# Kernel optimization log

Measured on AMD Instinct MI355X. Metric: run time of the kernel, lower is better.

Reference implementation:

```python
import jax, jax.numpy as jnp
import numpy as np

NUM_HEADS = 8


def setup_inputs() -> dict:
    key = jax.random.key(0)
    ks = jax.random.split(key, 12)
    b, c, h, w = 2, 256, 64, 64
    pe = 128  # palette_embed
    E = c
    s = 0.02
    return {
        "x": jax.random.normal(ks[0], (b, c, h, w), jnp.float32),
        "palette": jax.random.normal(ks[1], (b, pe, h, w), jnp.float32),
        "Wq": s * jax.random.normal(ks[2], (E, pe), jnp.float32),
        "bq": jnp.zeros((E,), jnp.float32),
        "Wk": s * jax.random.normal(ks[3], (E, E), jnp.float32),
        "bk": jnp.zeros((E,), jnp.float32),
        "Wv": s * jax.random.normal(ks[4], (E, E), jnp.float32),
        "bv": jnp.zeros((E,), jnp.float32),
        "Wo": s * jax.random.normal(ks[5], (E, E), jnp.float32),
        "bo": jnp.zeros((E,), jnp.float32),
    }


def reference(x, palette, Wq, bq, Wk, bk, Wv, bv, Wo, bo):
    b, c, h, w = x.shape
    E = c
    H = NUM_HEADS
    hd = E // H
    scale = hd ** -0.5

    # x: (b,c,h,w) -> (S, b, E)
    x_flat = x.reshape(b, c, h * w).transpose(2, 0, 1)
    k = x_flat @ Wk.T + bk  # (S, b, E)
    v = x_flat @ Wv.T + bv

    bp, cp, hp, wp = palette.shape
    p_flat = palette.reshape(bp, cp, hp * wp).transpose(2, 0, 1)  # (Sp, b, cp)
    q = p_flat @ Wq.T + bq  # (Sp, b, E)

    # Faithful to torch .view on (S,b,E)-contiguous tensors: flatten in that
    # memory order, then reshape to (b, L, H, hd) and move heads forward.
    def to_heads(t):
        return t.reshape(b, -1, H, hd).transpose(0, 2, 1, 3)  # (b, H, L, hd)

    qh, kh, vh = to_heads(q), to_heads(k), to_heads(v)

    scores = jnp.einsum("bhqd,bhkd->bhqk", qh, kh) * scale  # (b,H,Lq,Lk)
    attn = jax.nn.softmax(scores, axis=-1)
    out = jnp.einsum("bhqk,bhkd->bhqd", attn, vh)  # (b,H,Lq,hd)

    out = out.transpose(0, 2, 1, 3).reshape(b, -1, E)  # (b, Lq, E)
    out = out @ Wo.T + bo
    out = out.transpose(0, 2, 1).reshape(b, c, h, w)
    return x + out
```

## Files before the change

### kernel.cpp

```cpp
#include <hip/hip_runtime.h>

typedef unsigned int u32;
typedef unsigned short u16;
typedef __bf16 bf16x8 __attribute__((ext_vector_type(8)));
typedef float f32x4 __attribute__((ext_vector_type(4)));
typedef u32 u32x4 __attribute__((ext_vector_type(4)));
typedef u16 u16x4 __attribute__((ext_vector_type(4)));
typedef u16 u16x8 __attribute__((ext_vector_type(8)));

#define LOG2E 1.4426950408889634f
#define QSCALE 0.17677669529663687f

extern "C" __device__ float __ocml_native_exp2_f32(float);

__device__ __forceinline__ u16 f2bf(float f) {
  return __builtin_bit_cast(u16, static_cast<__bf16>(f));
}
__device__ __forceinline__ float bf2f(u16 u) {
  return __builtin_bit_cast(float, (u32)u << 16);
}
__device__ __forceinline__ u32 cvtpk(float lo, float hi) {
  u32 r;
  asm("v_cvt_pk_bf16_f32 %0, %1, %2" : "=v"(r) : "v"(lo), "v"(hi));
  return r;
}

__device__ __forceinline__ bf16x8 ldb8(const u16* p) {
  return __builtin_bit_cast(bf16x8, *(const u32x4*)p);
}

__device__ __forceinline__ f32x4 mfma16(bf16x8 a, bf16x8 b, f32x4 c) {
  return __builtin_amdgcn_mfma_f32_16x16x32_bf16(a, b, c, 0, 0, 0);
}

typedef __attribute__((address_space(3))) void lds_void;
typedef const __attribute__((address_space(1))) void gbl_void;
__device__ __forceinline__ void gl16(const void* g, void* l) {
  __builtin_amdgcn_global_load_lds((gbl_void*)g, (lds_void*)l, 16, 0, 0);
}

__global__ __launch_bounds__(256) void wconv(
    const float* __restrict__ wq, const float* __restrict__ wk,
    const float* __restrict__ wv, const float* __restrict__ wo,
    u16* __restrict__ dst) {
  int e4 = blockIdx.x * 256 + threadIdx.x;
  const float* src; int base;
  if (e4 < 8192)        { src = wq; base = 0; }
  else if (e4 < 24576)  { src = wk; base = 32768;  e4 -= 8192; }
  else if (e4 < 40960)  { src = wv; base = 98304;  e4 -= 24576; }
  else                  { src = wo; base = 163840; e4 -= 40960; }
  f32x4 v = *(const f32x4*)(src + e4 * 4);
  u16x4 r = { f2bf(v[0]), f2bf(v[1]), f2bf(v[2]), f2bf(v[3]) };
  *(u16x4*)(dst + base + e4 * 4) = r;
}

__global__ __launch_bounds__(256, 2) void qkv_proj(
    const float* __restrict__ x, const float* __restrict__ pal,
    const u16* __restrict__ wq, const u16* __restrict__ wk, const u16* __restrict__ wv,
    const float* __restrict__ bq, const float* __restrict__ bk, const float* __restrict__ bv,
    u16* __restrict__ qb, u16* __restrict__ kb, u16* __restrict__ vtg) {
  __shared__ alignas(16) u16 Xt[32 * 264];
  __shared__ alignas(16) u16 Pt[32 * 136];
  const int t = threadIdx.x;
  const int g0 = blockIdx.x * 32;
  const int s0 = g0 >> 1;
#pragma unroll
  for (int pass = 0; pass < 8; ++pass) {
    int c = pass * 256 + t;
    int row = c >> 2;
    int sc = (c & 3) * 4;
    f32x4 v = *(const f32x4*)(x + row * 4096 + s0 + sc);
#pragma unroll
    for (int i = 0; i < 4; ++i)
      Xt[(2 * (sc + i) + (row >> 8)) * 264 + (row & 255)] = f2bf(v[i]);
  }
#pragma unroll
  for (int pass = 0; pass < 4; ++pass) {
    int c = pass * 256 + t;
    int row = c >> 2;
    int sc = (c & 3) * 4;
    f32x4 v = *(const f32x4*)(pal + row * 4096 + s0 + sc);
#pragma unroll
    for (int i = 0; i < 4; ++i)
      Pt[(2 * (sc + i) + (row >> 7)) * 136 + (row & 127)] = f2bf(v[i]);
  }
  __syncthreads();

  const int lane = t & 63, w = t >> 6;
  const int c16 = lane & 15, g16 = lane >> 4;
  const int rtok = (w & 1) * 16 + c16;
  const int ntb = (w >> 1) * 8 + blockIdx.y * 4;
  const int B2 = g0 >> 12;
  const int l0 = (g0 & 4095) + (w & 1) * 16 + g16 * 4;

  bf16x8 ax[8], ap[4];
#pragma unroll
  for (int ks = 0; ks < 8; ++ks) ax[ks] = ldb8(&Xt[rtok * 264 + ks * 32 + g16 * 8]);
#pragma unroll
  for (int ks = 0; ks < 4; ++ks) ap[ks] = ldb8(&Pt[rtok * 136 + ks * 32 + g16 * 8]);

#pragma unroll 1
  for (int nt = ntb; nt < ntb + 4; ++nt) {
    const int e = nt * 16 + c16;
    const int hh = e >> 5, d = e & 31;
    const int bh = B2 * 8 + hh;
    f32x4 acc = {0.f, 0.f, 0.f, 0.f};
#pragma unroll
    for (int ks = 0; ks < 4; ++ks)
      acc = mfma16(ap[ks], ldb8(&wq[e * 128 + ks * 32 + g16 * 8]), acc);
    {
      float bb_ = bq[e];
      u16* dstq = qb + bh * 131072 + d;
#pragma unroll
      for (int j = 0; j < 4; ++j)
        dstq[(l0 + j) * 32] = f2bf((acc[j] + bb_) * (QSCALE * LOG2E));
    }
    acc = (f32x4){0.f, 0.f, 0.f, 0.f};
#pragma unroll
    for (int ks = 0; ks < 8; ++ks)
      acc = mfma16(ax[ks], ldb8(&wk[e * 256 + ks * 32 + g16 * 8]), acc);
    {
      float bb_ = bk[e];
      u16* dstk = kb + bh * 131072 + d;
#pragma unroll
      for (int j = 0; j < 4; ++j)
        dstk[(l0 + j) * 32] = f2bf(acc[j] + bb_);
    }
    acc = (f32x4){0.f, 0.f, 0.f, 0.f};
#pragma unroll
    for (int ks = 0; ks < 8; ++ks)
      acc = mfma16(ax[ks], ldb8(&wv[e * 256 + ks * 32 + g16 * 8]), acc);
    {
      float bb_ = bv[e];
      u16x4 pk = { f2bf(acc[0] + bb_), f2bf(acc[1] + bb_),
                   f2bf(acc[2] + bb_), f2bf(acc[3] + bb_) };
      *(u16x4*)&vtg[(bh * 32 + d) * 4096 + l0] = pk;
    }
  }
}

template <int SPLIT>
__global__ __launch_bounds__(256, 4) void attn(
    const u16* __restrict__ qb, const u16* __restrict__ kb,
    const u16* __restrict__ vtg, u16* __restrict__ po, float* __restrict__ plp) {
  __shared__ alignas(16) u16 Kl[2][64 * 32];
  __shared__ alignas(16) u16 Vl[2][32 * 64];
  const int t = threadIdx.x, lane = t & 63, w = t >> 6;
  const int c16 = lane & 15, g16 = lane >> 4;
  const int bh = blockIdx.x & 15;
  const int half = SPLIT ? ((blockIdx.x >> 4) & 1) : 0;
  const int qt = blockIdx.x >> (SPLIT ? 5 : 4);
  const int nIt = SPLIT ? 32 : 64;
  const u16* Qp = qb + bh * 131072;
  const int qrow0 = qt * 128 + w * 32;

  const int kr = t >> 2;
  const u16* ks0 = kb + bh * 131072 + half * 65536 + kr * 32 + (((t & 3) ^ (kr & 3)) * 8);
  const int vr = t >> 3;
  const u16* vs0 = vtg + bh * 131072 + vr * 4096 + half * 2048 + (((t & 7) ^ (vr & 7)) * 8);

  bf16x8 aq0 = ldb8(&Qp[(qrow0 + c16) * 32 + g16 * 8]);
  bf16x8 aq1 = ldb8(&Qp[(qrow0 + 16 + c16) * 32 + g16 * 8]);
  const u32 one2 = 0x3F803F80u;
  const bf16x8 ones = __builtin_bit_cast(bf16x8, (u32x4){one2, one2, one2, one2});

  f32x4 oa00 = {0.f, 0.f, 0.f, 0.f}, oa01 = {0.f, 0.f, 0.f, 0.f};
  f32x4 oa10 = {0.f, 0.f, 0.f, 0.f}, oa11 = {0.f, 0.f, 0.f, 0.f};
  f32x4 la0 = {0.f, 0.f, 0.f, 0.f}, la1 = {0.f, 0.f, 0.f, 0.f};

  gl16(ks0, &Kl[0][t * 8]);
  gl16(vs0, &Vl[0][t * 8]);
  __syncthreads();

  int cur = 0;
  for (int it = 0; it < nIt; ++it) {
    if (it + 1 < nIt) {
      gl16(ks0 + (it + 1) * 2048, &Kl[cur ^ 1][t * 8]);
      gl16(vs0 + (it + 1) * 64, &Vl[cur ^ 1][t * 8]);
    }
    f32x4 s0[4], s1[4];
    __builtin_amdgcn_s_setprio(1);
#pragma unroll
    for (int rt = 0; rt < 4; ++rt) {
      bf16x8 ka = ldb8(&Kl[cur][(rt * 16 + c16) * 32 + ((g16 ^ (c16 & 3)) * 8)]);
      s0[rt] = mfma16(ka, aq0, (f32x4){0.f, 0.f, 0.f, 0.f});
      s1[rt] = mfma16(ka, aq1, (f32x4){0.f, 0.f, 0.f, 0.f});
    }
    __builtin_amdgcn_s_setprio(0);
    u32 pk01[2][4], pk23[2][4];
#pragma unroll
    for (int rt = 0; rt < 4; ++rt) {
      pk01[0][rt] = cvtpk(__ocml_native_exp2_f32(s0[rt][0]), __ocml_native_exp2_f32(s0[rt][1]));
      pk23[0][rt] = cvtpk(__ocml_native_exp2_f32(s0[rt][2]), __ocml_native_exp2_f32(s0[rt][3]));
      pk01[1][rt] = cvtpk(__ocml_native_exp2_f32(s1[rt][0]), __ocml_native_exp2_f32(s1[rt][1]));
      pk23[1][rt] = cvtpk(__ocml_native_exp2_f32(s1[rt][2]), __ocml_native_exp2_f32(s1[rt][3]));
    }
#pragma unroll
    for (int ksl = 0; ksl < 2; ++ksl) {
      u32 A0 = pk01[0][ksl * 2], B0 = pk01[0][ksl * 2 + 1];
      u32 C0 = pk23[0][ksl * 2], D0 = pk23[0][ksl * 2 + 1];
      u32 A1 = pk01[1][ksl * 2], B1 = pk01[1][ksl * 2 + 1];
      u32 C1 = pk23[1][ksl * 2], D1 = pk23[1][ksl * 2 + 1];
      asm("v_permlane32_swap_b32 %0, %1\n\t"
          "v_permlane16_swap_b32 %0, %1" : "+v"(A0), "+v"(B0));
      asm("v_permlane32_swap_b32 %0, %1\n\t"
          "v_permlane16_swap_b32 %0, %1" : "+v"(C0), "+v"(D0));
      asm("v_permlane32_swap_b32 %0, %1\n\t"
          "v_permlane16_swap_b32 %0, %1" : "+v"(A1), "+v"(B1));
      asm("v_permlane32_swap_b32 %0, %1\n\t"
          "v_permlane16_swap_b32 %0, %1" : "+v"(C1), "+v"(D1));
      bf16x8 pa0 = __builtin_bit_cast(bf16x8, (u32x4){A0, C0, B0, D0});
      bf16x8 pa1 = __builtin_bit_cast(bf16x8, (u32x4){A1, C1, B1, D1});
      const int sw = ((ksl * 4 + g16) ^ (c16 & 7)) * 8;
      bf16x8 bv0 = ldb8(&Vl[cur][c16 * 64 + sw]);
      bf16x8 bv1 = ldb8(&Vl[cur][(16 + c16) * 64 + sw]);
      __builtin_amdgcn_s_setprio(1);
      oa00 = mfma16(pa0, bv0, oa00);
      oa01 = mfma16(pa0, bv1, oa01);
      la0  = mfma16(pa0, ones, la0);
      oa10 = mfma16(pa1, bv0, oa10);
      oa11 = mfma16(pa1, bv1, oa11);
      la1  = mfma16(pa1, ones, la1);
      __builtin_amdgcn_s_setprio(0);
    }
    __syncthreads();
    cur ^= 1;
  }
  if (SPLIT) {
    const int hb = half * 16 + bh;
#pragma unroll
    for (int j = 0; j < 4; ++j) {
      int q0 = qrow0 + g16 * 4 + j;
      int q1 = q0 + 16;
      po[hb * 131072 + q0 * 32 + c16] = f2bf(oa00[j]);
      po[hb * 131072 + q0 * 32 + 16 + c16] = f2bf(oa01[j]);
      po[hb * 131072 + q1 * 32 + c16] = f2bf(oa10[j]);
      po[hb * 131072 + q1 * 32 + 16 + c16] = f2bf(oa11[j]);
    }
    if (c16 == 0) {
#pragma unroll
      for (int j = 0; j < 4; ++j) {
        plp[hb * 4096 + qrow0 + g16 * 4 + j] = la0[j];
        plp[hb * 4096 + qrow0 + 16 + g16 * 4 + j] = la1[j];
      }
    }
  } else {
#pragma unroll
    for (int j = 0; j < 4; ++j) {
      float inv0 = 1.0f / la0[j];
      float inv1 = 1.0f / la1[j];
      int q0 = qrow0 + g16 * 4 + j;
      int q1 = q0 + 16;
      po[bh * 131072 + q0 * 32 + c16] = f2bf(oa00[j] * inv0);
      po[bh * 131072 + q0 * 32 + 16 + c16] = f2bf(oa01[j] * inv0);
      po[bh * 131072 + q1 * 32 + c16] = f2bf(oa10[j] * inv1);
      po[bh * 131072 + q1 * 32 + 16 + c16] = f2bf(oa11[j] * inv1);
    }
  }
}

__global__ __launch_bounds__(256) void reduce2(
    const u16* __restrict__ po, const float* __restrict__ plp,
    u16* __restrict__ ob) {
  const int idx = blockIdx.x * 256 + threadIdx.x;
  const int gq = idx >> 2, oct = (idx & 3) * 8;
  const float inv = 1.0f / (plp[gq] + plp[65536 + gq]);
  u16x8 a = *(const u16x8*)&po[gq * 32 + oct];
  u16x8 b = *(const u16x8*)&po[2097152 + gq * 32 + oct];
  u16x8 o;
#pragma unroll
  for (int i = 0; i < 8; ++i) o[i] = f2bf((bf2f(a[i]) + bf2f(b[i])) * inv);
  *(u16x8*)&ob[gq * 32 + oct] = o;
}

__global__ __launch_bounds__(256, 2) void oproj(
    const u16* __restrict__ ob, const u16* __restrict__ wo,
    const float* __restrict__ bo, const float* __restrict__ x,
    float* __restrict__ out) {
  const int t = threadIdx.x, lane = t & 63, w = t >> 6;
  const int c16 = lane & 15, g16 = lane >> 4;
  const int g0 = blockIdx.x * 32;
  const int B2 = g0 >> 12;
  const int lrow = (g0 & 4095) + (w & 1) * 16;
  bf16x8 ao[8];
#pragma unroll
  for (int ks = 0; ks < 8; ++ks)
    ao[ks] = ldb8(&ob[(B2 * 8 + ks) * 131072 + (lrow + c16) * 32 + g16 * 8]);
  const int ntb = (w >> 1) * 8 + blockIdx.y * 4;
#pragma unroll 1
  for (int nt = ntb; nt < ntb + 4; ++nt) {
    const int e = nt * 16 + c16;
    f32x4 acc = {0.f, 0.f, 0.f, 0.f};
#pragma unroll
    for (int ks = 0; ks < 8; ++ks)
      acc = mfma16(ao[ks], ldb8(&wo[e * 256 + ks * 32 + g16 * 8]), acc);
    const float boe = bo[e];
    const int lb = lrow + g16 * 4;
    const f32x4 xr = *(const f32x4*)(x + (B2 * 256 + e) * 4096 + lb);
    f32x4 o4 = { acc[0] + boe + xr[0], acc[1] + boe + xr[1],
                 acc[2] + boe + xr[2], acc[3] + boe + xr[3] };
    *(f32x4*)(out + (B2 * 256 + e) * 4096 + lb) = o4;
  }
}

extern "C" void kernel_launch(void* const* d_in, const int* in_sizes, int n_in,
                              void* d_out, int out_size, void* d_ws, size_t ws_size,
                              hipStream_t stream) {
  const float* x   = (const float*)d_in[0];
  const float* pal = (const float*)d_in[1];
  const float* Wq  = (const float*)d_in[2];
  const float* bq  = (const float*)d_in[3];
  const float* Wk  = (const float*)d_in[4];
  const float* bk  = (const float*)d_in[5];
  const float* Wv  = (const float*)d_in[6];
  const float* bv  = (const float*)d_in[7];
  const float* Wo  = (const float*)d_in[8];
  const float* bo  = (const float*)d_in[9];

  char* ws = (char*)d_ws;
  u16* qb  = (u16*)(ws);
  u16* kb  = (u16*)(ws + (4u << 20));
  u16* vtg = (u16*)(ws + (8u << 20));
  u16* obuf= (u16*)(ws + (12u << 20));
  u16* wbf = (u16*)(ws + (16u << 20));
  u16* po  = (u16*)(ws + (17u << 20));
  float* plp = (float*)(ws + (25u << 20));
  u16* wqb = wbf;
  u16* wkb = wbf + 32768;
  u16* wvb = wbf + 98304;
  u16* wob = wbf + 163840;

  wconv<<<224, 256, 0, stream>>>(Wq, Wk, Wv, Wo, wbf);
  qkv_proj<<<dim3(256, 2), 256, 0, stream>>>(x, pal, wqb, wkb, wvb, bq, bk, bv, qb, kb, vtg);
  if (ws_size >= (26u << 20)) {
    attn<1><<<1024, 256, 0, stream>>>(qb, kb, vtg, po, plp);
    reduce2<<<1024, 256, 0, stream>>>(po, plp, obuf);
  } else {
    attn<0><<<512, 256, 0, stream>>>(qb, kb, vtg, obuf, nullptr);
  }
  oproj<<<dim3(256, 2), 256, 0, stream>>>(obuf, wob, bo, x, (float*)d_out);
}
```

Measured before the change: 97.97 us.

## Split attention keys four ways, fuse split reduction into oproj, widen qkv blocks

The attention kernel is templated on a key-split count and launched with a 4-way split (2048 blocks), with an occupancy hint of 8 blocks per CU, so more blocks keep the GPU busy. The separate reduce2 kernel is removed. oproj now combines the per-split partial outputs and row sums itself while loading its A operand, which saves one launch and one intermediate buffer round-trip. qkv_proj is changed to 512-thread blocks that cover all output columns instead of two y-blocks, so the x and palette tiles are staged once per token block. The cost is more partial-result traffic, because both oproj y-blocks re-read all splits. The 4-way path also needs a larger workspace, otherwise it falls back to the 2-way or unsplit path.

```diff
diff --git a/kernel.cpp b/kernel.cpp
--- a/kernel.cpp
+++ b/kernel.cpp
@@ -54,7 +54,7 @@
   *(u16x4*)(dst + base + e4 * 4) = r;
 }
 
-__global__ __launch_bounds__(256, 2) void qkv_proj(
+__global__ __launch_bounds__(512, 2) void qkv_proj(
     const float* __restrict__ x, const float* __restrict__ pal,
     const u16* __restrict__ wq, const u16* __restrict__ wk, const u16* __restrict__ wv,
     const float* __restrict__ bq, const float* __restrict__ bk, const float* __restrict__ bv,
@@ -65,8 +65,8 @@
   const int g0 = blockIdx.x * 32;
   const int s0 = g0 >> 1;
 #pragma unroll
-  for (int pass = 0; pass < 8; ++pass) {
-    int c = pass * 256 + t;
+  for (int pass = 0; pass < 4; ++pass) {
+    int c = pass * 512 + t;
     int row = c >> 2;
     int sc = (c & 3) * 4;
     f32x4 v = *(const f32x4*)(x + row * 4096 + s0 + sc);
@@ -75,8 +75,8 @@
       Xt[(2 * (sc + i) + (row >> 8)) * 264 + (row & 255)] = f2bf(v[i]);
   }
 #pragma unroll
-  for (int pass = 0; pass < 4; ++pass) {
-    int c = pass * 256 + t;
+  for (int pass = 0; pass < 2; ++pass) {
+    int c = pass * 512 + t;
     int row = c >> 2;
     int sc = (c & 3) * 4;
     f32x4 v = *(const f32x4*)(pal + row * 4096 + s0 + sc);
@@ -89,7 +89,7 @@
   const int lane = t & 63, w = t >> 6;
   const int c16 = lane & 15, g16 = lane >> 4;
   const int rtok = (w & 1) * 16 + c16;
-  const int ntb = (w >> 1) * 8 + blockIdx.y * 4;
+  const int ntb = (w >> 1) * 4;
   const int B2 = g0 >> 12;
   const int l0 = (g0 & 4095) + (w & 1) * 16 + g16 * 4;
 
@@ -139,8 +139,8 @@
   }
 }
 
-template <int SPLIT>
-__global__ __launch_bounds__(256, 4) void attn(
+template <int NSPLIT>
+__global__ __launch_bounds__(256, 8) void attn(
     const u16* __restrict__ qb, const u16* __restrict__ kb,
     const u16* __restrict__ vtg, u16* __restrict__ po, float* __restrict__ plp) {
   __shared__ alignas(16) u16 Kl[2][64 * 32];
@@ -148,16 +148,18 @@
   const int t = threadIdx.x, lane = t & 63, w = t >> 6;
   const int c16 = lane & 15, g16 = lane >> 4;
   const int bh = blockIdx.x & 15;
-  const int half = SPLIT ? ((blockIdx.x >> 4) & 1) : 0;
-  const int qt = blockIdx.x >> (SPLIT ? 5 : 4);
-  const int nIt = SPLIT ? 32 : 64;
+  const int half = (NSPLIT > 1) ? ((blockIdx.x >> 4) & (NSPLIT - 1)) : 0;
+  const int qt = blockIdx.x >> (NSPLIT == 4 ? 6 : (NSPLIT == 2 ? 5 : 4));
+  const int nIt = 64 / NSPLIT;
   const u16* Qp = qb + bh * 131072;
   const int qrow0 = qt * 128 + w * 32;
 
   const int kr = t >> 2;
-  const u16* ks0 = kb + bh * 131072 + half * 65536 + kr * 32 + (((t & 3) ^ (kr & 3)) * 8);
+  const u16* ks0 = kb + bh * 131072 + half * (65536 / (NSPLIT / 2 + (NSPLIT == 1)))
+                   + kr * 32 + (((t & 3) ^ (kr & 3)) * 8);
   const int vr = t >> 3;
-  const u16* vs0 = vtg + bh * 131072 + vr * 4096 + half * 2048 + (((t & 7) ^ (vr & 7)) * 8);
+  const u16* vs0 = vtg + bh * 131072 + vr * 4096 + half * (4096 / NSPLIT)
+                   + (((t & 7) ^ (vr & 7)) * 8);
 
   bf16x8 aq0 = ldb8(&Qp[(qrow0 + c16) * 32 + g16 * 8]);
   bf16x8 aq1 = ldb8(&Qp[(qrow0 + 16 + c16) * 32 + g16 * 8]);
@@ -226,7 +228,7 @@
     __syncthreads();
     cur ^= 1;
   }
-  if (SPLIT) {
+  if (NSPLIT > 1) {
     const int hb = half * 16 + bh;
 #pragma unroll
     for (int j = 0; j < 4; ++j) {
@@ -259,33 +261,41 @@
   }
 }
 
-__global__ __launch_bounds__(256) void reduce2(
+template <int NSPLIT>
+__global__ __launch_bounds__(256, 2) void oproj(
     const u16* __restrict__ po, const float* __restrict__ plp,
-    u16* __restrict__ ob) {
-  const int idx = blockIdx.x * 256 + threadIdx.x;
-  const int gq = idx >> 2, oct = (idx & 3) * 8;
-  const float inv = 1.0f / (plp[gq] + plp[65536 + gq]);
-  u16x8 a = *(const u16x8*)&po[gq * 32 + oct];
-  u16x8 b = *(const u16x8*)&po[2097152 + gq * 32 + oct];
-  u16x8 o;
-#pragma unroll
-  for (int i = 0; i < 8; ++i) o[i] = f2bf((bf2f(a[i]) + bf2f(b[i])) * inv);
-  *(u16x8*)&ob[gq * 32 + oct] = o;
-}
-
-__global__ __launch_bounds__(256, 2) void oproj(
-    const u16* __restrict__ ob, const u16* __restrict__ wo,
-    const float* __restrict__ bo, const float* __restrict__ x,
-    float* __restrict__ out) {
+    const u16* __restrict__ wo, const float* __restrict__ bo,
+    const float* __restrict__ x, float* __restrict__ out) {
   const int t = threadIdx.x, lane = t & 63, w = t >> 6;
   const int c16 = lane & 15, g16 = lane >> 4;
   const int g0 = blockIdx.x * 32;
   const int B2 = g0 >> 12;
   const int lrow = (g0 & 4095) + (w & 1) * 16;
+  const int q = lrow + c16;
   bf16x8 ao[8];
 #pragma unroll
-  for (int ks = 0; ks < 8; ++ks)
-    ao[ks] = ldb8(&ob[(B2 * 8 + ks) * 131072 + (lrow + c16) * 32 + g16 * 8]);
+  for (int ks = 0; ks < 8; ++ks) {
+    const int bh = B2 * 8 + ks;
+    if (NSPLIT == 1) {
+      ao[ks] = ldb8(&po[bh * 131072 + q * 32 + g16 * 8]);
+    } else {
+      float acc8[8] = {0.f, 0.f, 0.f, 0.f, 0.f, 0.f, 0.f, 0.f};
+      float lsum = 0.f;
+#pragma unroll
+      for (int h = 0; h < NSPLIT; ++h) {
+        lsum += plp[h * 65536 + bh * 4096 + q];
+        u16x8 pv = *(const u16x8*)&po[h * 2097152 + bh * 131072 + q * 32 + g16 * 8];
+#pragma unroll
+        for (int i = 0; i < 8; ++i) acc8[i] += bf2f(pv[i]);
+      }
+      const float inv = 1.0f / lsum;
+      u32 w0 = cvtpk(acc8[0] * inv, acc8[1] * inv);
+      u32 w1 = cvtpk(acc8[2] * inv, acc8[3] * inv);
+      u32 w2 = cvtpk(acc8[4] * inv, acc8[5] * inv);
+      u32 w3 = cvtpk(acc8[6] * inv, acc8[7] * inv);
+      ao[ks] = __builtin_bit_cast(bf16x8, (u32x4){w0, w1, w2, w3});
+    }
+  }
   const int ntb = (w >> 1) * 8 + blockIdx.y * 4;
 #pragma unroll 1
   for (int nt = ntb; nt < ntb + 4; ++nt) {
@@ -324,19 +334,23 @@
   u16* obuf= (u16*)(ws + (12u << 20));
   u16* wbf = (u16*)(ws + (16u << 20));
   u16* po  = (u16*)(ws + (17u << 20));
-  float* plp = (float*)(ws + (25u << 20));
   u16* wqb = wbf;
   u16* wkb = wbf + 32768;
   u16* wvb = wbf + 98304;
   u16* wob = wbf + 163840;
 
   wconv<<<224, 256, 0, stream>>>(Wq, Wk, Wv, Wo, wbf);
-  qkv_proj<<<dim3(256, 2), 256, 0, stream>>>(x, pal, wqb, wkb, wvb, bq, bk, bv, qb, kb, vtg);
-  if (ws_size >= (26u << 20)) {
-    attn<1><<<1024, 256, 0, stream>>>(qb, kb, vtg, po, plp);
-    reduce2<<<1024, 256, 0, stream>>>(po, plp, obuf);
+  qkv_proj<<<256, 512, 0, stream>>>(x, pal, wqb, wkb, wvb, bq, bk, bv, qb, kb, vtg);
+  if (ws_size >= (34u << 20)) {
+    float* plp = (float*)(ws + (33u << 20));
+    attn<4><<<2048, 256, 0, stream>>>(qb, kb, vtg, po, plp);
+    oproj<4><<<dim3(256, 2), 256, 0, stream>>>(po, plp, wob, bo, x, (float*)d_out);
+  } else if (ws_size >= (26u << 20)) {
+    float* plp = (float*)(ws + (25u << 20));
+    attn<2><<<1024, 256, 0, stream>>>(qb, kb, vtg, po, plp);
+    oproj<2><<<dim3(256, 2), 256, 0, stream>>>(po, plp, wob, bo, x, (float*)d_out);
   } else {
-    attn<0><<<512, 256, 0, stream>>>(qb, kb, vtg, obuf, nullptr);
-  }
-  oproj<<<dim3(256, 2), 256, 0, stream>>>(obuf, wob, bo, x, (float*)d_out);
-}
+    attn<1><<<512, 256, 0, stream>>>(qb, kb, vtg, obuf, nullptr);
+    oproj<1><<<dim3(256, 2), 256, 0, stream>>>(obuf, nullptr, wob, bo, x, (float*)d_out);
+  }
+}
```

Result: slower. 212.7 us (+117.1%).
